# Kernel tuning notes

Hardware: AMD Instinct MI355X
Metric: run time of the kernel (lower is better)

## Reference

```python
import jax, jax.numpy as jnp
import numpy as np

N_NODES = 50000
N_EDGES = 600000
D = 128
N_GRAPHS = 64


def setup_inputs() -> dict:
    key = jax.random.key(0)
    ks = jax.random.split(key, 16)
    x = jax.random.normal(ks[0], (N_NODES, D), dtype=jnp.float32)
    edge_index = jax.random.randint(ks[1], (2, N_EDGES), 0, N_NODES, dtype=jnp.int64)
    batch = jnp.sort(jax.random.randint(ks[2], (N_NODES,), 0, N_GRAPHS, dtype=jnp.int64))
    s = 1.0 / np.sqrt(D)
    def lin(k, out_d, in_d):
        return jax.random.uniform(k, (out_d, in_d), jnp.float32, -s, s)
    inp = {"x": x, "edge_index": edge_index, "batch": batch}
    for i, base in zip(range(3), (3, 6, 9)):
        inp[f"W_rel{i+1}"] = lin(ks[base], D, D)
        inp[f"b_rel{i+1}"] = jax.random.uniform(ks[base + 1], (D,), jnp.float32, -s, s)
        inp[f"W_root{i+1}"] = lin(ks[base + 2], D, D)
    s5 = 1.0 / np.sqrt(5)
    inp["W1"] = lin(ks[12], 5, D)
    inp["b1"] = jax.random.uniform(ks[13], (5,), jnp.float32, -s, s)
    inp["W2"] = jax.random.uniform(ks[14], (1, 5), jnp.float32, -s5, s5)
    inp["b2"] = jax.random.uniform(ks[15], (1,), jnp.float32, -s5, s5)
    return inp


def graph_conv(x, src, dst, W_rel, b_rel, W_root):
    # PyG GraphConv: out_i = W_root x_i + W_rel * sum_{j->i} x_j + b_rel
    agg = jax.ops.segment_sum(x[src], dst, num_segments=N_NODES)  # [N, D]
    return agg @ W_rel.T + b_rel + x @ W_root.T


def reference(x, edge_index, batch,
              W_rel1, b_rel1, W_root1,
              W_rel2, b_rel2, W_root2,
              W_rel3, b_rel3, W_root3,
              W1, b1, W2, b2):
    src, dst = edge_index[0], edge_index[1]
    h = jax.nn.relu(graph_conv(x, src, dst, W_rel1, b_rel1, W_root1))
    h = jax.nn.relu(graph_conv(h, src, dst, W_rel2, b_rel2, W_root2))
    h = graph_conv(h, src, dst, W_rel3, b_rel3, W_root3)
    # global max pool over graphs
    g = jax.ops.segment_max(h, batch, num_segments=N_GRAPHS)  # [G, D]
    out = jax.nn.relu(g @ W1.T + b1) @ W2.T + b2  # [G, 1]
    return out
```

## Files before the change

### kernel.cpp

```cpp
#include <hip/hip_runtime.h>
#include <float.h>

#define N_NODES 50000
#define N_EDGES 600000
#define D 128
#define N_GRAPHS 64
#define SCAN_T 256
#define SCAN_NBLK ((N_NODES + SCAN_T - 1) / SCAN_T)

typedef __attribute__((ext_vector_type(8))) short short8;
typedef __attribute__((ext_vector_type(4))) float floatx4;

__device__ inline float bf2f(unsigned short h) {
    return __uint_as_float((unsigned)h << 16);
}
__device__ inline unsigned short f2bf(float f) {
    unsigned u = __float_as_uint(f);
    return (unsigned short)((u + 0x7fffu + ((u >> 16) & 1u)) >> 16);
}


__global__ void prep(int* __restrict__ deg, float* __restrict__ g) {
    int i = blockIdx.x * 256 + threadIdx.x;
    if (i < N_NODES) deg[i] = 0;
    if (i < N_GRAPHS * D) g[i] = -FLT_MAX;
}


__global__ void cast_all(const float4* __restrict__ x, ushort4* __restrict__ xb, int n4,
                         const float* __restrict__ Wr0, const float* __restrict__ Wo0,
                         const float* __restrict__ Wr1, const float* __restrict__ Wo1,
                         const float* __restrict__ Wr2, const float* __restrict__ Wo2,
                         unsigned short* __restrict__ B0, unsigned short* __restrict__ B1,
                         unsigned short* __restrict__ B2) {
    int idx = blockIdx.x * 256 + threadIdx.x;
    if (idx < n4) {
        float4 v = x[idx];
        ushort4 o;
        o.x = f2bf(v.x); o.y = f2bf(v.y); o.z = f2bf(v.z); o.w = f2bf(v.w);
        xb[idx] = o;
        return;
    }
    int w = idx - n4;
    if (w >= 3 * 128 * 256) return;
    int l = w >> 15;
    int r = w & 32767;
    int o = r >> 8, k = r & 255;
    const float* Wr = (l == 0) ? Wr0 : (l == 1) ? Wr1 : Wr2;
    const float* Wo = (l == 0) ? Wo0 : (l == 1) ? Wo1 : Wo2;
    unsigned short* B = (l == 0) ? B0 : (l == 1) ? B1 : B2;
    float v = (k < 128) ? Wr[o * 128 + k] : Wo[o * 128 + (k - 128)];
    B[r] = f2bf(v);
}


__global__ void count_deg(const int* __restrict__ ei, int* __restrict__ deg) {
    int e = blockIdx.x * 256 + threadIdx.x;
    if (e < N_EDGES) atomicAdd(&deg[ei[N_EDGES + e]], 1);
}

__global__ __launch_bounds__(SCAN_T) void block_sum(const int* __restrict__ deg,
                                                    int* __restrict__ blockSums) {
    __shared__ int s[SCAN_T];
    int tid = threadIdx.x;
    int i = blockIdx.x * SCAN_T + tid;
    s[tid] = (i < N_NODES) ? deg[i] : 0;
    __syncthreads();
    for (int off = SCAN_T / 2; off > 0; off >>= 1) {
        if (tid < off) s[tid] += s[tid + off];
        __syncthreads();
    }
    if (tid == 0) blockSums[blockIdx.x] = s[0];
}

__global__ __launch_bounds__(SCAN_T) void scan_blocks(const int* __restrict__ blockSums,
                                                      int* __restrict__ blockOff,
                                                      int* __restrict__ row_start) {
    __shared__ int s[SCAN_T];
    int tid = threadIdx.x;
    int v = (tid < SCAN_NBLK) ? blockSums[tid] : 0;
    s[tid] = v;
    __syncthreads();
    for (int off = 1; off < SCAN_T; off <<= 1) {
        int t = (tid >= off) ? s[tid - off] : 0;
        __syncthreads();
        s[tid] += t;
        __syncthreads();
    }
    if (tid < SCAN_NBLK) blockOff[tid] = s[tid] - v;
    if (tid == SCAN_T - 1) row_start[N_NODES] = s[tid];
}

__global__ __launch_bounds__(SCAN_T) void scan_write(const int* __restrict__ deg,
                                                     const int* __restrict__ blockOff,
                                                     int* __restrict__ row_start,
                                                     int* __restrict__ cursor) {
    __shared__ int s[SCAN_T];
    int tid = threadIdx.x;
    int i = blockIdx.x * SCAN_T + tid;
    int v = (i < N_NODES) ? deg[i] : 0;
    s[tid] = v;
    __syncthreads();
    for (int off = 1; off < SCAN_T; off <<= 1) {
        int t = (tid >= off) ? s[tid - off] : 0;
        __syncthreads();
        s[tid] += t;
        __syncthreads();
    }
    if (i < N_NODES) {
        int rs = blockOff[blockIdx.x] + s[tid] - v;
        row_start[i] = rs;
        cursor[i]    = rs;
    }
}

__global__ void fill_csr(const int* __restrict__ ei, int* __restrict__ cursor,
                         int* __restrict__ csr_src) {
    int e = blockIdx.x * 256 + threadIdx.x;
    if (e < N_EDGES) {
        int dst = ei[N_EDGES + e];
        int pos = atomicAdd(&cursor[dst], 1);
        csr_src[pos] = ei[e];
    }
}


__global__ __launch_bounds__(256) void csr_gather_bf16(
    const unsigned short* __restrict__ xb, const int* __restrict__ row_start,
    const int* __restrict__ csr_src, unsigned short* __restrict__ aggb)
{
    int node = blockIdx.x * 8 + (threadIdx.x >> 5);
    int lane = threadIdx.x & 31;
    if (node >= N_NODES) return;
    int beg = row_start[node];
    int end = row_start[node + 1];

    float a0 = 0.f, a1 = 0.f, a2 = 0.f, a3 = 0.f;
    for (int base = beg; base < end; base += 32) {
        int n = end - base; if (n > 32) n = 32;
        int idx = (lane < n) ? csr_src[base + lane] : 0;
        int j = 0;
        for (; j + 3 < n; j += 4) {
            int s0 = __shfl(idx, j,     32);
            int s1 = __shfl(idx, j + 1, 32);
            int s2 = __shfl(idx, j + 2, 32);
            int s3 = __shfl(idx, j + 3, 32);
            ushort4 u0 = *(const ushort4*)(xb + (size_t)s0 * D + lane * 4);
            ushort4 u1 = *(const ushort4*)(xb + (size_t)s1 * D + lane * 4);
            ushort4 u2 = *(const ushort4*)(xb + (size_t)s2 * D + lane * 4);
            ushort4 u3 = *(const ushort4*)(xb + (size_t)s3 * D + lane * 4);
            a0 += bf2f(u0.x) + bf2f(u1.x) + bf2f(u2.x) + bf2f(u3.x);
            a1 += bf2f(u0.y) + bf2f(u1.y) + bf2f(u2.y) + bf2f(u3.y);
            a2 += bf2f(u0.z) + bf2f(u1.z) + bf2f(u2.z) + bf2f(u3.z);
            a3 += bf2f(u0.w) + bf2f(u1.w) + bf2f(u2.w) + bf2f(u3.w);
        }
        for (; j < n; ++j) {
            int s0 = __shfl(idx, j, 32);
            ushort4 u0 = *(const ushort4*)(xb + (size_t)s0 * D + lane * 4);
            a0 += bf2f(u0.x); a1 += bf2f(u0.y); a2 += bf2f(u0.z); a3 += bf2f(u0.w);
        }
    }
    ushort4 r;
    r.x = f2bf(a0); r.y = f2bf(a1); r.z = f2bf(a2); r.w = f2bf(a3);
    *(ushort4*)(aggb + (size_t)node * D + lane * 4) = r;
}


__global__ __launch_bounds__(256) void gemm_mfma(
    const unsigned short* __restrict__ aggb, const unsigned short* __restrict__ xb,
    const unsigned short* __restrict__ Bb, const float* __restrict__ bias,
    unsigned short* __restrict__ Ob, int relu)
{
    int tid  = threadIdx.x;
    int wave = tid >> 6;
    int lane = tid & 63;
    int m    = lane & 15;
    int quad = lane >> 4;
    int row0 = blockIdx.x * 64 + wave * 16;

    floatx4 acc[8];
#pragma unroll
    for (int t = 0; t < 8; ++t) acc[t] = (floatx4){0.f, 0.f, 0.f, 0.f};

    int arow = row0 + m;
    if (arow > N_NODES - 1) arow = N_NODES - 1;

#pragma unroll
    for (int ks = 0; ks < 8; ++ks) {
        int k0 = ks * 32;
        const unsigned short* Asrc = (k0 < 128) ? aggb : xb;
        int kk = k0 & 127;
        short8 a = *(const short8*)(Asrc + (size_t)arow * 128 + kk + quad * 8);
#pragma unroll
        for (int t = 0; t < 8; ++t) {
            short8 b = *(const short8*)(Bb + (size_t)(t * 16 + m) * 256 + k0 + quad * 8);
            acc[t] = __builtin_amdgcn_mfma_f32_16x16x32_bf16(a, b, acc[t], 0, 0, 0);
        }
    }

#pragma unroll
    for (int t = 0; t < 8; ++t) {
        int col = t * 16 + m;
        float bv = bias[col];
#pragma unroll
        for (int r = 0; r < 4; ++r) {
            int row = row0 + quad * 4 + r;
            if (row >= N_NODES) continue;
            float v = acc[t][r] + bv;
            if (relu) v = fmaxf(v, 0.f);
            Ob[(size_t)row * D + col] = f2bf(v);
        }
    }
}


__global__ __launch_bounds__(256) void gemm_pool(
    const unsigned short* __restrict__ aggb, const unsigned short* __restrict__ xb,
    const unsigned short* __restrict__ Bb, const float* __restrict__ bias,
    const int* __restrict__ batch, float* __restrict__ g)
{
    __shared__ float Cs[64][129];
    int tid  = threadIdx.x;
    int wave = tid >> 6;
    int lane = tid & 63;
    int m    = lane & 15;
    int quad = lane >> 4;
    int row0 = blockIdx.x * 64;
    int trow0 = row0 + wave * 16;

    floatx4 acc[8];
#pragma unroll
    for (int t = 0; t < 8; ++t) acc[t] = (floatx4){0.f, 0.f, 0.f, 0.f};

    int arow = trow0 + m;
    if (arow > N_NODES - 1) arow = N_NODES - 1;

#pragma unroll
    for (int ks = 0; ks < 8; ++ks) {
        int k0 = ks * 32;
        const unsigned short* Asrc = (k0 < 128) ? aggb : xb;
        int kk = k0 & 127;
        short8 a = *(const short8*)(Asrc + (size_t)arow * 128 + kk + quad * 8);
#pragma unroll
        for (int t = 0; t < 8; ++t) {
            short8 b = *(const short8*)(Bb + (size_t)(t * 16 + m) * 256 + k0 + quad * 8);
            acc[t] = __builtin_amdgcn_mfma_f32_16x16x32_bf16(a, b, acc[t], 0, 0, 0);
        }
    }

#pragma unroll
    for (int t = 0; t < 8; ++t) {
        int col = t * 16 + m;
        float bv = bias[col];
#pragma unroll
        for (int r = 0; r < 4; ++r)
            Cs[wave * 16 + quad * 4 + r][col] = acc[t][r] + bv;
    }
    __syncthreads();

    int col  = tid & 127;
    int rbeg = (tid >> 7) * 32;
    float cur = -FLT_MAX;
    int curb  = -1;
    for (int r = rbeg; r < rbeg + 32; ++r) {
        int grow = row0 + r;
        if (grow >= N_NODES) break;
        int b = batch[grow];
        if (b != curb) {
            if (curb >= 0) {
                float* ad = &g[curb * D + col];
                if (cur >= 0.f) atomicMax((int*)ad, __float_as_int(cur));
                else            atomicMin((unsigned int*)ad, __float_as_uint(cur));
            }
            curb = b;
            cur = -FLT_MAX;
        }
        cur = fmaxf(cur, Cs[r][col]);
    }
    if (curb >= 0) {
        float* ad = &g[curb * D + col];
        if (cur >= 0.f) atomicMax((int*)ad, __float_as_int(cur));
        else            atomicMin((unsigned int*)ad, __float_as_uint(cur));
    }
}


__global__ void mlp_head(const float* __restrict__ g,
                         const float* __restrict__ W1, const float* __restrict__ b1,
                         const float* __restrict__ W2, const float* __restrict__ b2,
                         float* __restrict__ out) {
    int gi = threadIdx.x;
    if (gi >= N_GRAPHS) return;
    float h[5];
#pragma unroll
    for (int j = 0; j < 5; ++j) {
        float acc = b1[j];
        for (int k = 0; k < D; ++k) acc += g[gi * D + k] * W1[j * D + k];
        h[j] = fmaxf(acc, 0.f);
    }
    float o = b2[0];
#pragma unroll
    for (int j = 0; j < 5; ++j) o += h[j] * W2[j];
    out[gi] = o;
}

extern "C" void kernel_launch(void* const* d_in, const int* in_sizes, int n_in,
                              void* d_out, int out_size, void* d_ws, size_t ws_size,
                              hipStream_t stream) {
    const float* x     = (const float*)d_in[0];
    const int*   ei    = (const int*)d_in[1];
    const int*   batch = (const int*)d_in[2];
    const float* Wrel[3]  = {(const float*)d_in[3], (const float*)d_in[6], (const float*)d_in[9]};
    const float* brel[3]  = {(const float*)d_in[4], (const float*)d_in[7], (const float*)d_in[10]};
    const float* Wroot[3] = {(const float*)d_in[5], (const float*)d_in[8], (const float*)d_in[11]};
    const float* W1 = (const float*)d_in[12];
    const float* b1 = (const float*)d_in[13];
    const float* W2 = (const float*)d_in[14];
    const float* b2 = (const float*)d_in[15];
    float* out = (float*)d_out;

    char* ws = (char*)d_ws;
    const size_t nodeB16 = (size_t)N_NODES * D * sizeof(unsigned short);
    unsigned short* xb   = (unsigned short*)(ws);
    unsigned short* aggb = (unsigned short*)(ws + nodeB16);
    unsigned short* hb1  = (unsigned short*)(ws + 2 * nodeB16);
    unsigned short* hb2  = (unsigned short*)(ws + 3 * nodeB16);
    char* p = ws + 4 * nodeB16;
    unsigned short* Bb0 = (unsigned short*)p;   p += 128 * 256 * sizeof(unsigned short);
    unsigned short* Bb1 = (unsigned short*)p;   p += 128 * 256 * sizeof(unsigned short);
    unsigned short* Bb2 = (unsigned short*)p;   p += 128 * 256 * sizeof(unsigned short);
    float* g        = (float*)p;                p += N_GRAPHS * D * sizeof(float);
    int*   deg      = (int*)p;                  p += N_NODES * sizeof(int);
    int*   row_start= (int*)p;                  p += (N_NODES + 1) * sizeof(int);
    int*   cursor   = (int*)p;                  p += N_NODES * sizeof(int);
    int*   csr_src  = (int*)p;                  p += N_EDGES * sizeof(int);
    int*   blockSums= (int*)p;                  p += SCAN_NBLK * sizeof(int);
    int*   blockOff = (int*)p;                  p += SCAN_NBLK * sizeof(int);

    prep<<<SCAN_NBLK, 256, 0, stream>>>(deg, g);
    count_deg<<<(N_EDGES + 255) / 256, 256, 0, stream>>>(ei, deg);
    block_sum<<<SCAN_NBLK, SCAN_T, 0, stream>>>(deg, blockSums);
    scan_blocks<<<1, SCAN_T, 0, stream>>>(blockSums, blockOff, row_start);
    scan_write<<<SCAN_NBLK, SCAN_T, 0, stream>>>(deg, blockOff, row_start, cursor);
    fill_csr<<<(N_EDGES + 255) / 256, 256, 0, stream>>>(ei, cursor, csr_src);

    const int n4 = N_NODES * D / 4;
    const int cast_total = n4 + 3 * 128 * 256;
    cast_all<<<(cast_total + 255) / 256, 256, 0, stream>>>(
        (const float4*)x, (ushort4*)xb, n4,
        Wrel[0], Wroot[0], Wrel[1], Wroot[1], Wrel[2], Wroot[2],
        Bb0, Bb1, Bb2);

    const int ggrid = (N_NODES + 7) / 8;
    const int mgrid = (N_NODES + 63) / 64;

    csr_gather_bf16<<<ggrid, 256, 0, stream>>>(xb, row_start, csr_src, aggb);
    gemm_mfma<<<mgrid, 256, 0, stream>>>(aggb, xb, Bb0, brel[0], hb1, 1);

    csr_gather_bf16<<<ggrid, 256, 0, stream>>>(hb1, row_start, csr_src, aggb);
    gemm_mfma<<<mgrid, 256, 0, stream>>>(aggb, hb1, Bb1, brel[1], hb2, 1);

    csr_gather_bf16<<<ggrid, 256, 0, stream>>>(hb2, row_start, csr_src, aggb);
    gemm_pool<<<mgrid, 256, 0, stream>>>(aggb, hb2, Bb2, brel[2], batch, g);

    mlp_head<<<1, 64, 0, stream>>>(g, W1, b1, W2, b2, out);
}
```

Measured before the change: 365.1 us.

## Stage GEMM weights in LDS, unroll gather by 8, and vectorize pooling

The GEMM kernels now preload all A fragments into registers and stage the weight matrix in shared memory in two halves, so each wave reads it from LDS instead of issuing redundant global loads. The CSR gather loop is unrolled by 8 to put more independent loads in flight. In gemm_pool, batch ids are cached in shared memory and the max-pool loops over graph ids with a branch-free select instead of per-row branching. This adds LDS use and extra barriers, which may lower occupancy. It also assumes batch is sorted, which holds for the test inputs.

```diff
diff --git a/kernel.cpp b/kernel.cpp
--- a/kernel.cpp
+++ b/kernel.cpp
@@ -140,11 +140,31 @@
         int n = end - base; if (n > 32) n = 32;
         int idx = (lane < n) ? csr_src[base + lane] : 0;
         int j = 0;
+        for (; j + 7 < n; j += 8) {
+            int s0 = __shfl(idx, j,     32); int s1 = __shfl(idx, j + 1, 32);
+            int s2 = __shfl(idx, j + 2, 32); int s3 = __shfl(idx, j + 3, 32);
+            int s4 = __shfl(idx, j + 4, 32); int s5 = __shfl(idx, j + 5, 32);
+            int s6 = __shfl(idx, j + 6, 32); int s7 = __shfl(idx, j + 7, 32);
+            ushort4 u0 = *(const ushort4*)(xb + (size_t)s0 * D + lane * 4);
+            ushort4 u1 = *(const ushort4*)(xb + (size_t)s1 * D + lane * 4);
+            ushort4 u2 = *(const ushort4*)(xb + (size_t)s2 * D + lane * 4);
+            ushort4 u3 = *(const ushort4*)(xb + (size_t)s3 * D + lane * 4);
+            ushort4 u4 = *(const ushort4*)(xb + (size_t)s4 * D + lane * 4);
+            ushort4 u5 = *(const ushort4*)(xb + (size_t)s5 * D + lane * 4);
+            ushort4 u6 = *(const ushort4*)(xb + (size_t)s6 * D + lane * 4);
+            ushort4 u7 = *(const ushort4*)(xb + (size_t)s7 * D + lane * 4);
+            a0 += bf2f(u0.x) + bf2f(u1.x) + bf2f(u2.x) + bf2f(u3.x)
+                + bf2f(u4.x) + bf2f(u5.x) + bf2f(u6.x) + bf2f(u7.x);
+            a1 += bf2f(u0.y) + bf2f(u1.y) + bf2f(u2.y) + bf2f(u3.y)
+                + bf2f(u4.y) + bf2f(u5.y) + bf2f(u6.y) + bf2f(u7.y);
+            a2 += bf2f(u0.z) + bf2f(u1.z) + bf2f(u2.z) + bf2f(u3.z)
+                + bf2f(u4.z) + bf2f(u5.z) + bf2f(u6.z) + bf2f(u7.z);
+            a3 += bf2f(u0.w) + bf2f(u1.w) + bf2f(u2.w) + bf2f(u3.w)
+                + bf2f(u4.w) + bf2f(u5.w) + bf2f(u6.w) + bf2f(u7.w);
+        }
         for (; j + 3 < n; j += 4) {
-            int s0 = __shfl(idx, j,     32);
-            int s1 = __shfl(idx, j + 1, 32);
-            int s2 = __shfl(idx, j + 2, 32);
-            int s3 = __shfl(idx, j + 3, 32);
+            int s0 = __shfl(idx, j,     32); int s1 = __shfl(idx, j + 1, 32);
+            int s2 = __shfl(idx, j + 2, 32); int s3 = __shfl(idx, j + 3, 32);
             ushort4 u0 = *(const ushort4*)(xb + (size_t)s0 * D + lane * 4);
             ushort4 u1 = *(const ushort4*)(xb + (size_t)s1 * D + lane * 4);
             ushort4 u2 = *(const ushort4*)(xb + (size_t)s2 * D + lane * 4);
@@ -166,11 +186,27 @@
 }
 
 
+__device__ inline void stage_b_half(unsigned short* sB, const unsigned short* __restrict__ Bb,
+                                    int tid, int h) {
+#pragma unroll
+    for (int i = 0; i < 8; ++i) {
+        int flat = tid + i * 256;
+        int fi = flat >> 6, ln = flat & 63;
+        int mm = ln & 15, qq = ln >> 4;
+        int ksL = fi >> 3, tt = fi & 7;
+        short8 v = *(const short8*)(Bb + (size_t)(tt * 16 + mm) * 256
+                                    + (h * 4 + ksL) * 32 + qq * 8);
+        *(short8*)(sB + (size_t)flat * 8) = v;
+    }
+}
+
+
 __global__ __launch_bounds__(256) void gemm_mfma(
     const unsigned short* __restrict__ aggb, const unsigned short* __restrict__ xb,
     const unsigned short* __restrict__ Bb, const float* __restrict__ bias,
     unsigned short* __restrict__ Ob, int relu)
 {
+    __shared__ unsigned short sB[16384];
     int tid  = threadIdx.x;
     int wave = tid >> 6;
     int lane = tid & 63;
@@ -178,25 +214,39 @@
     int quad = lane >> 4;
     int row0 = blockIdx.x * 64 + wave * 16;
 
-    floatx4 acc[8];
-#pragma unroll
-    for (int t = 0; t < 8; ++t) acc[t] = (floatx4){0.f, 0.f, 0.f, 0.f};
-
     int arow = row0 + m;
     if (arow > N_NODES - 1) arow = N_NODES - 1;
 
+    short8 af[8];
 #pragma unroll
     for (int ks = 0; ks < 8; ++ks) {
-        int k0 = ks * 32;
-        const unsigned short* Asrc = (k0 < 128) ? aggb : xb;
-        int kk = k0 & 127;
-        short8 a = *(const short8*)(Asrc + (size_t)arow * 128 + kk + quad * 8);
+        const unsigned short* Asrc = (ks < 4) ? aggb : xb;
+        af[ks] = *(const short8*)(Asrc + (size_t)arow * 128 + (ks & 3) * 32 + quad * 8);
+    }
+
+    floatx4 acc[8];
+#pragma unroll
+    for (int t = 0; t < 8; ++t) acc[t] = (floatx4){0.f, 0.f, 0.f, 0.f};
+
+    stage_b_half(sB, Bb, tid, 0);
+    __syncthreads();
+#pragma unroll
+    for (int ksL = 0; ksL < 4; ++ksL)
 #pragma unroll
         for (int t = 0; t < 8; ++t) {
-            short8 b = *(const short8*)(Bb + (size_t)(t * 16 + m) * 256 + k0 + quad * 8);
-            acc[t] = __builtin_amdgcn_mfma_f32_16x16x32_bf16(a, b, acc[t], 0, 0, 0);
-        }
-    }
+            short8 b = *(const short8*)(sB + (size_t)((ksL * 8 + t) * 64 + lane) * 8);
+            acc[t] = __builtin_amdgcn_mfma_f32_16x16x32_bf16(af[ksL], b, acc[t], 0, 0, 0);
+        }
+    __syncthreads();
+    stage_b_half(sB, Bb, tid, 1);
+    __syncthreads();
+#pragma unroll
+    for (int ksL = 0; ksL < 4; ++ksL)
+#pragma unroll
+        for (int t = 0; t < 8; ++t) {
+            short8 b = *(const short8*)(sB + (size_t)((ksL * 8 + t) * 64 + lane) * 8);
+            acc[t] = __builtin_amdgcn_mfma_f32_16x16x32_bf16(af[4 + ksL], b, acc[t], 0, 0, 0);
+        }
 
 #pragma unroll
     for (int t = 0; t < 8; ++t) {
@@ -214,39 +264,61 @@
 }
 
 
+struct PoolShared {
+    union {
+        unsigned short b[16384];
+        float c[64 * 129];
+    };
+};
+
 __global__ __launch_bounds__(256) void gemm_pool(
     const unsigned short* __restrict__ aggb, const unsigned short* __restrict__ xb,
     const unsigned short* __restrict__ Bb, const float* __restrict__ bias,
     const int* __restrict__ batch, float* __restrict__ g)
 {
-    __shared__ float Cs[64][129];
+    __shared__ PoolShared sh;
+    __shared__ int bl[64];
     int tid  = threadIdx.x;
     int wave = tid >> 6;
     int lane = tid & 63;
     int m    = lane & 15;
     int quad = lane >> 4;
     int row0 = blockIdx.x * 64;
-    int trow0 = row0 + wave * 16;
+
+    int arow = row0 + wave * 16 + m;
+    if (arow > N_NODES - 1) arow = N_NODES - 1;
+
+    short8 af[8];
+#pragma unroll
+    for (int ks = 0; ks < 8; ++ks) {
+        const unsigned short* Asrc = (ks < 4) ? aggb : xb;
+        af[ks] = *(const short8*)(Asrc + (size_t)arow * 128 + (ks & 3) * 32 + quad * 8);
+    }
 
     floatx4 acc[8];
 #pragma unroll
     for (int t = 0; t < 8; ++t) acc[t] = (floatx4){0.f, 0.f, 0.f, 0.f};
 
-    int arow = trow0 + m;
-    if (arow > N_NODES - 1) arow = N_NODES - 1;
-
-#pragma unroll
-    for (int ks = 0; ks < 8; ++ks) {
-        int k0 = ks * 32;
-        const unsigned short* Asrc = (k0 < 128) ? aggb : xb;
-        int kk = k0 & 127;
-        short8 a = *(const short8*)(Asrc + (size_t)arow * 128 + kk + quad * 8);
+    stage_b_half(sh.b, Bb, tid, 0);
+    __syncthreads();
+#pragma unroll
+    for (int ksL = 0; ksL < 4; ++ksL)
 #pragma unroll
         for (int t = 0; t < 8; ++t) {
-            short8 b = *(const short8*)(Bb + (size_t)(t * 16 + m) * 256 + k0 + quad * 8);
-            acc[t] = __builtin_amdgcn_mfma_f32_16x16x32_bf16(a, b, acc[t], 0, 0, 0);
-        }
-    }
+            short8 b = *(const short8*)(sh.b + (size_t)((ksL * 8 + t) * 64 + lane) * 8);
+            acc[t] = __builtin_amdgcn_mfma_f32_16x16x32_bf16(af[ksL], b, acc[t], 0, 0, 0);
+        }
+    __syncthreads();
+    stage_b_half(sh.b, Bb, tid, 1);
+    __syncthreads();
+#pragma unroll
+    for (int ksL = 0; ksL < 4; ++ksL)
+#pragma unroll
+        for (int t = 0; t < 8; ++t) {
+            short8 b = *(const short8*)(sh.b + (size_t)((ksL * 8 + t) * 64 + lane) * 8);
+            acc[t] = __builtin_amdgcn_mfma_f32_16x16x32_bf16(af[4 + ksL], b, acc[t], 0, 0, 0);
+        }
+    __syncthreads();
 
 #pragma unroll
     for (int t = 0; t < 8; ++t) {
@@ -254,33 +326,31 @@
         float bv = bias[col];
 #pragma unroll
         for (int r = 0; r < 4; ++r)
-            Cs[wave * 16 + quad * 4 + r][col] = acc[t][r] + bv;
-    }
-    __syncthreads();
-
+            sh.c[(wave * 16 + quad * 4 + r) * 129 + col] = acc[t][r] + bv;
+    }
+    if (tid < 64) {
+        int grow = row0 + tid;
+        bl[tid] = (grow < N_NODES) ? batch[grow] : -1;
+    }
+    __syncthreads();
+
+    int nvalid = min(64, N_NODES - row0);
+    int b0 = bl[0], b1 = bl[nvalid - 1];
     int col  = tid & 127;
     int rbeg = (tid >> 7) * 32;
-    float cur = -FLT_MAX;
-    int curb  = -1;
-    for (int r = rbeg; r < rbeg + 32; ++r) {
-        int grow = row0 + r;
-        if (grow >= N_NODES) break;
-        int b = batch[grow];
-        if (b != curb) {
-            if (curb >= 0) {
-                float* ad = &g[curb * D + col];
-                if (cur >= 0.f) atomicMax((int*)ad, __float_as_int(cur));
-                else            atomicMin((unsigned int*)ad, __float_as_uint(cur));
-            }
-            curb = b;
-            cur = -FLT_MAX;
-        }
-        cur = fmaxf(cur, Cs[r][col]);
-    }
-    if (curb >= 0) {
-        float* ad = &g[curb * D + col];
-        if (cur >= 0.f) atomicMax((int*)ad, __float_as_int(cur));
-        else            atomicMin((unsigned int*)ad, __float_as_uint(cur));
+    for (int gg = b0; gg <= b1; ++gg) {
+        float cur = -FLT_MAX;
+#pragma unroll
+        for (int r = 0; r < 32; ++r) {
+            int rr = rbeg + r;
+            float v = (bl[rr] == gg) ? sh.c[rr * 129 + col] : -FLT_MAX;
+            cur = fmaxf(cur, v);
+        }
+        if (cur > -FLT_MAX) {
+            float* ad = &g[gg * D + col];
+            if (cur >= 0.f) atomicMax((int*)ad, __float_as_int(cur));
+            else            atomicMin((unsigned int*)ad, __float_as_uint(cur));
+        }
     }
 }
 
```

Measured after the change: 309.5 us. 15.2% less time.
